# Optimization experiments

Hardware: AMD Instinct MI355X
Metric: run time of the kernel (lower is better)

Reference implementation:

```python
import jax, jax.numpy as jnp
import numpy as np

K = 2
N_NODES = 100_000
N_EDGES = 1_600_000
STATIC_F = 16
DYN_F = 32
EDGE_F = 8
IN_F = EDGE_F + 2 * STATIC_F + 2 * DYN_F  # 104
HID_F = 2 * DYN_F  # 64


def setup_inputs() -> dict:
    key = jax.random.key(0)
    ks = jax.random.split(key, 9)
    x_s = jax.random.normal(ks[0], (N_NODES, STATIC_F), dtype=jnp.float32)
    x_t = jax.random.normal(ks[1], (N_NODES, DYN_F), dtype=jnp.float32)
    edge_index = jax.random.randint(ks[2], (2, N_EDGES), 0, N_NODES, dtype=jnp.int64 if jax.config.jax_enable_x64 else jnp.int32)
    edge_attr = jax.random.normal(ks[3], (N_EDGES, EDGE_F), dtype=jnp.float32)
    W1 = jax.random.normal(ks[4], (IN_F, HID_F), dtype=jnp.float32) / np.sqrt(IN_F)
    b1 = jnp.zeros((HID_F,), dtype=jnp.float32)
    W2 = jax.random.normal(ks[5], (HID_F, DYN_F), dtype=jnp.float32) / np.sqrt(HID_F)
    b2 = jnp.zeros((DYN_F,), dtype=jnp.float32)
    F = jax.random.normal(ks[6], (K + 1, DYN_F, DYN_F), dtype=jnp.float32) / np.sqrt(DYN_F)
    return {"x_s": x_s, "x_t": x_t, "edge_index": edge_index, "edge_attr": edge_attr,
            "W1": W1, "b1": b1, "W2": W2, "b2": b2, "F": F}


def reference(x_s, x_t, edge_index, edge_attr, W1, b1, W2, b2, F):
    row, col = edge_index[0], edge_index[1]
    num_nodes = x_t.shape[0]
    # filter_matrix[0] (Linear, no bias); F[k] stored as [in, out]
    out = x_t @ F[0]
    xs_row = x_s[row]  # static gathers are loop-invariant
    xs_col = x_s[col]
    for k in range(K):
        mask = jnp.sum(out, axis=1) != 0  # [N]
        edge_mask = (mask[row] | mask[col]).astype(out.dtype)[:, None]  # [E,1]
        out_row = out[row]
        out_col = out[col]
        e_ij = jnp.concatenate([xs_row, xs_col, out_row, out_col, edge_attr], axis=1)  # [E,104]
        w_ij = jax.nn.relu(e_ij @ W1 + b1) @ W2 + b2  # [E,32]
        # normalize per edge; NaN (zero-norm) -> 0, matching masked_fill_
        nrm = jnp.linalg.norm(w_ij, axis=1, keepdims=True)
        w_ij = jnp.where(nrm > 0, w_ij / jnp.where(nrm > 0, nrm, 1.0), 0.0)
        # with_gradient: (x_j - x_i) * w_ij; zero out edges failing the mask
        shift = (out_col - out_row) * w_ij * edge_mask
        scattered = jax.ops.segment_sum(shift, col, num_segments=num_nodes)
        out = out + scattered @ F[k + 1]
    return out
```

## Files before the change

### kernel.cpp

```cpp
#include <hip/hip_runtime.h>

#define NN 100000
#define NE 1600000
#define SF 16
#define DF 32
#define EFT 8
#define HF 64

typedef __attribute__((ext_vector_type(8))) short short8;
typedef __attribute__((ext_vector_type(4))) float floatx4;

__device__ inline unsigned short f2bf(float f) {
  union { float f; unsigned int u; } v; v.f = f;
  unsigned int u = v.u + 0x7FFFu + ((v.u >> 16) & 1u);
  return (unsigned short)(u >> 16);
}
__device__ inline float bf2f(unsigned short h) {
  union { unsigned int u; float f; } v; v.u = ((unsigned int)h) << 16;
  return v.f;
}

__global__ __launch_bounds__(256) void hist_kernel(const int* __restrict__ ei,
                                                   int* __restrict__ deg) {
  int e = blockIdx.x * 256 + threadIdx.x;
  if (e < NE) atomicAdd(&deg[ei[NE + e]], 1);
}

__global__ __launch_bounds__(256) void scan1_kernel(const int* __restrict__ deg,
                                                    int* __restrict__ cur,
                                                    int* __restrict__ bsums) {
  __shared__ int ts[256];
  int tid = threadIdx.x;
  int base = blockIdx.x * 1024 + tid * 4;
  int v[4];
#pragma unroll
  for (int q = 0; q < 4; ++q) v[q] = (base + q < NN) ? deg[base + q] : 0;
  int s = v[0] + v[1] + v[2] + v[3];
  ts[tid] = s;
  __syncthreads();
  for (int off = 1; off < 256; off <<= 1) {
    int t = (tid >= off) ? ts[tid - off] : 0;
    __syncthreads();
    ts[tid] += t;
    __syncthreads();
  }
  int excl = ts[tid] - s;
  if (tid == 255) bsums[blockIdx.x] = ts[255];
  int run = excl;
#pragma unroll
  for (int q = 0; q < 4; ++q) {
    if (base + q < NN) cur[base + q] = run;
    run += v[q];
  }
}

__global__ void scan2_kernel(int* __restrict__ bsums, int nb) {
  int acc = 0;
  for (int i = 0; i < nb; ++i) { int t = bsums[i]; bsums[i] = acc; acc += t; }
}

__global__ __launch_bounds__(256) void scan3_kernel(int* __restrict__ cur,
                                                    const int* __restrict__ bsums) {
  int i = blockIdx.x * 256 + threadIdx.x;
  if (i < NN) cur[i] += bsums[i >> 10];
}

__global__ __launch_bounds__(256) void fill_kernel(const int* __restrict__ ei,
                                                   const float* __restrict__ ea,
                                                   int* __restrict__ cur,
                                                   int* __restrict__ row_s,
                                                   int* __restrict__ col_s,
                                                   unsigned short* __restrict__ ea_s) {
  int e = blockIdx.x * 256 + threadIdx.x;
  if (e >= NE) return;
  int r = ei[e];
  int c = ei[NE + e];
  int pos = atomicAdd(&cur[c], 1);
  row_s[pos] = r;
  col_s[pos] = c;
  const float4* p = (const float4*)(ea + (size_t)e * EFT);
  float4 v0 = p[0], v1 = p[1];
  short8 ev;
  ev[0] = (short)f2bf(v0.x); ev[1] = (short)f2bf(v0.y);
  ev[2] = (short)f2bf(v0.z); ev[3] = (short)f2bf(v0.w);
  ev[4] = (short)f2bf(v1.x); ev[5] = (short)f2bf(v1.y);
  ev[6] = (short)f2bf(v1.z); ev[7] = (short)f2bf(v1.w);
  *(short8*)(ea_s + (size_t)pos * 8) = ev;
}

__global__ __launch_bounds__(256) void wpre_kernel(const float* __restrict__ W1,
                                                   unsigned short* __restrict__ WpreT) {
  int id = blockIdx.x * 256 + threadIdx.x;
  if (id >= 128 * 64) return;
  int col = id >> 6, k = id & 63;
  int j = col & 63;
  bool bh = col >= 64;
  float v = 0.f;
  if (k < 16) v = W1[((bh ? 16 : 0) + k) * HF + j];
  else if (k < 48) v = W1[((bh ? 64 : 32) + (k - 16)) * HF + j];
  WpreT[col * 64 + k] = f2bf(v);
}

__global__ __launch_bounds__(256) void init_kernel(
    const float* __restrict__ x_t, const float* __restrict__ F0,
    float* __restrict__ out, unsigned short* __restrict__ outb,
    float* __restrict__ sums) {
  int n = blockIdx.x * 256 + threadIdx.x;
  if (n >= NN) return;
  float x[DF];
  const float4* xr = reinterpret_cast<const float4*>(x_t + (size_t)n * DF);
#pragma unroll
  for (int q = 0; q < 8; ++q) {
    float4 v = xr[q];
    x[4*q+0]=v.x; x[4*q+1]=v.y; x[4*q+2]=v.z; x[4*q+3]=v.w;
  }
  float4* orow = reinterpret_cast<float4*>(out + (size_t)n * DF);
  unsigned short* ob = outb + (size_t)n * DF;
  float s = 0.f;
#pragma unroll
  for (int q = 0; q < 8; ++q) {
    float4 acc = {0.f, 0.f, 0.f, 0.f};
#pragma unroll
    for (int i = 0; i < DF; ++i) {
      float xi = x[i];
      acc.x = fmaf(xi, F0[i*DF + 4*q+0], acc.x);
      acc.y = fmaf(xi, F0[i*DF + 4*q+1], acc.y);
      acc.z = fmaf(xi, F0[i*DF + 4*q+2], acc.z);
      acc.w = fmaf(xi, F0[i*DF + 4*q+3], acc.w);
    }
    orow[q] = acc;
    s += acc.x + acc.y + acc.z + acc.w;
    ushort4 pk = {f2bf(acc.x), f2bf(acc.y), f2bf(acc.z), f2bf(acc.w)};
    *(ushort4*)(ob + 4*q) = pk;
  }
  sums[n] = s;
}

__global__ __launch_bounds__(256, 4) void pre_kernel(
    const float* __restrict__ x_s, const unsigned short* __restrict__ outb,
    const unsigned short* __restrict__ WpreT, unsigned short* __restrict__ ABh) {
  __shared__ unsigned short wlds[128][72];
  int tid = threadIdx.x;
  for (int t = tid; t < 128 * 8; t += 256) {
    int colr = t >> 3, kc = t & 7;
    short8 v = *(const short8*)(WpreT + colr * 64 + kc * 8);
    *(short8*)(&wlds[colr][kc * 8]) = v;
  }
  __syncthreads();

  int lcol = tid & 15, kgrp = (tid >> 4) & 3, wid = tid >> 6;
  int nodebase = blockIdx.x * 64 + wid * 16;
  int nodeA = nodebase + lcol;

  short8 a0 = {0,0,0,0,0,0,0,0}, a1 = {0,0,0,0,0,0,0,0};
  if (nodeA < NN) {
    const unsigned short* obp = outb + (size_t)nodeA * DF;
    if (kgrp == 0) {
      const float4* p = (const float4*)(x_s + (size_t)nodeA * SF);
      float4 v0 = p[0], v1 = p[1];
      a0[0]=(short)f2bf(v0.x); a0[1]=(short)f2bf(v0.y);
      a0[2]=(short)f2bf(v0.z); a0[3]=(short)f2bf(v0.w);
      a0[4]=(short)f2bf(v1.x); a0[5]=(short)f2bf(v1.y);
      a0[6]=(short)f2bf(v1.z); a0[7]=(short)f2bf(v1.w);
      a1 = *(const short8*)(obp + 16);
    } else if (kgrp == 1) {
      const float4* p = (const float4*)(x_s + (size_t)nodeA * SF);
      float4 v0 = p[2], v1 = p[3];
      a0[0]=(short)f2bf(v0.x); a0[1]=(short)f2bf(v0.y);
      a0[2]=(short)f2bf(v0.z); a0[3]=(short)f2bf(v0.w);
      a0[4]=(short)f2bf(v1.x); a0[5]=(short)f2bf(v1.y);
      a0[6]=(short)f2bf(v1.z); a0[7]=(short)f2bf(v1.w);
      a1 = *(const short8*)(obp + 24);
    } else if (kgrp == 2) {
      a0 = *(const short8*)(obp + 0);
    } else {
      a0 = *(const short8*)(obp + 8);
    }
  }

  floatx4 acc[8];
#pragma unroll
  for (int nt = 0; nt < 8; ++nt) {
    short8 b0 = *(const short8*)(&wlds[nt * 16 + lcol][kgrp * 8]);
    short8 b1 = *(const short8*)(&wlds[nt * 16 + lcol][32 + kgrp * 8]);
    floatx4 c = {0.f, 0.f, 0.f, 0.f};
    c = __builtin_amdgcn_mfma_f32_16x16x32_bf16(a0, b0, c, 0, 0, 0);
    c = __builtin_amdgcn_mfma_f32_16x16x32_bf16(a1, b1, c, 0, 0, 0);
    acc[nt] = c;
  }

#pragma unroll
  for (int rr = 0; rr < 4; ++rr) {
    int node = nodebase + kgrp * 4 + rr;
    if (node < NN) {
      unsigned short* dst = ABh + (size_t)node * 128;
#pragma unroll
      for (int nt = 0; nt < 8; ++nt)
        dst[nt * 16 + lcol] = f2bf(acc[nt][rr]);
    }
  }
}

__global__ __launch_bounds__(256, 4) void edge_kernel(
    const unsigned short* __restrict__ ABh, const unsigned short* __restrict__ outb,
    const float* __restrict__ sums, const unsigned short* __restrict__ ea_s,
    const int* __restrict__ row_s, const int* __restrict__ col_s,
    const float* __restrict__ W1, const float* __restrict__ b1,
    const float* __restrict__ W2, const float* __restrict__ b2,
    float* __restrict__ scattered) {
  __shared__ union { unsigned short h[256][72]; float sh[256][33]; } u;
  __shared__ int scol[256];
  __shared__ int srow[256];
  __shared__ union { float msk[256]; struct { unsigned short l0[256], l1[256]; } seg; } vv;
  __shared__ int wbase[4];
  __shared__ int cnt;

  int tid = threadIdx.x;
  int bbase = blockIdx.x * 256;
  int i = bbase + tid;
  if (tid == 0) cnt = 0;
  int lcol = tid & 15;
  int kgrp = (tid >> 4) & 3;
  int wid = tid >> 6;

  short8 w2f[2][2];
#pragma unroll
  for (int kt = 0; kt < 2; ++kt)
#pragma unroll
    for (int nt = 0; nt < 2; ++nt) {
#pragma unroll
      for (int q = 0; q < 8; ++q)
        w2f[kt][nt][q] = (short)f2bf(W2[(kt*32 + kgrp*8 + q) * DF + nt*16 + lcol]);
    }
  float b2c0 = b2[lcol], b2c1 = b2[16 + lcol];

  if (i < NE) {
    int r = row_s[i];
    int c = col_s[i];
    scol[tid] = c;
    srow[tid] = r;
    float s_r = sums[r], s_c = sums[c];
    vv.msk[tid] = (s_r == 0.f && s_c == 0.f) ? 0.f : 1.f;
    float eav[8];
    {
      short8 ev = *(const short8*)(ea_s + (size_t)i * 8);
#pragma unroll
      for (int t = 0; t < 8; ++t) eav[t] = bf2f((unsigned short)ev[t]);
    }
    const unsigned short* ar = ABh + (size_t)r * 128;
    const unsigned short* bc = ABh + (size_t)c * 128 + 64;
#pragma unroll 1
    for (int ch = 0; ch < 4; ++ch) {
      short8 a0 = *(const short8*)(ar + ch*16);
      short8 a1 = *(const short8*)(ar + ch*16 + 8);
      short8 c0 = *(const short8*)(bc + ch*16);
      short8 c1 = *(const short8*)(bc + ch*16 + 8);
      short8 p0, p1;
#pragma unroll
      for (int j = 0; j < 16; ++j) {
        float cj = b1[ch*16 + j];
#pragma unroll
        for (int t = 0; t < 8; ++t)
          cj = fmaf(eav[t], W1[(96 + t) * HF + ch*16 + j], cj);
        float av = bf2f((unsigned short)(j < 8 ? a0[j] : a1[j-8]));
        float bv = bf2f((unsigned short)(j < 8 ? c0[j] : c1[j-8]));
        float hv = fmaxf(av + bv + cj, 0.f);
        unsigned short hb = f2bf(hv);
        if (j < 8) p0[j] = (short)hb; else p1[j-8] = (short)hb;
      }
      *(short8*)(&u.h[tid][ch*16]) = p0;
      *(short8*)(&u.h[tid][ch*16 + 8]) = p1;
    }
  } else {
    scol[tid] = -1;
    srow[tid] = 0;
    vv.msk[tid] = 0.f;
  }
  __syncthreads();

  floatx4 acc[4][2];
#pragma unroll
  for (int g = 0; g < 4; ++g) {
    int erow = wid*64 + g*16 + lcol;
    short8 a0 = *(const short8*)(&u.h[erow][kgrp*8]);
    short8 a1 = *(const short8*)(&u.h[erow][32 + kgrp*8]);
    floatx4 c0 = {b2c0, b2c0, b2c0, b2c0};
    floatx4 c1 = {b2c1, b2c1, b2c1, b2c1};
    c0 = __builtin_amdgcn_mfma_f32_16x16x32_bf16(a0, w2f[0][0], c0, 0, 0, 0);
    c0 = __builtin_amdgcn_mfma_f32_16x16x32_bf16(a1, w2f[1][0], c0, 0, 0, 0);
    c1 = __builtin_amdgcn_mfma_f32_16x16x32_bf16(a0, w2f[0][1], c1, 0, 0, 0);
    c1 = __builtin_amdgcn_mfma_f32_16x16x32_bf16(a1, w2f[1][1], c1, 0, 0, 0);
    acc[g][0] = c0;
    acc[g][1] = c1;
  }
  __syncthreads();

#pragma unroll
  for (int g = 0; g < 4; ++g) {
    float nsq[4];
#pragma unroll
    for (int rr = 0; rr < 4; ++rr)
      nsq[rr] = acc[g][0][rr]*acc[g][0][rr] + acc[g][1][rr]*acc[g][1][rr];
#pragma unroll
    for (int mm = 1; mm <= 8; mm <<= 1) {
#pragma unroll
      for (int rr = 0; rr < 4; ++rr)
        nsq[rr] += __shfl_xor(nsq[rr], mm, 64);
    }
#pragma unroll
    for (int rr = 0; rr < 4; ++rr) {
      int e = wid*64 + g*16 + kgrp*4 + rr;
      if (bbase + e < NE) {
        float ms = (nsq[rr] > 0.f) ? rsqrtf(nsq[rr]) : 0.f;
        ms *= vv.msk[e];
        int r2 = srow[e];
        int c2 = scol[e];
        float ar0 = bf2f(outb[(size_t)r2*DF + lcol]);
        float ar1 = bf2f(outb[(size_t)r2*DF + 16 + lcol]);
        float bc0 = bf2f(outb[(size_t)c2*DF + lcol]);
        float bc1 = bf2f(outb[(size_t)c2*DF + 16 + lcol]);
        u.sh[e][lcol]      = (bc0 - ar0) * acc[g][0][rr] * ms;
        u.sh[e][16 + lcol] = (bc1 - ar1) * acc[g][1][rr] * ms;
      }
    }
  }
  __syncthreads();

  int c_self = scol[tid];
  bool head = (c_self >= 0) && (tid == 0 || scol[tid-1] != c_self);
  unsigned long long m = __ballot(head);
  int lane = tid & 63;
  if (lane == 0) wbase[wid] = atomicAdd(&cnt, (int)__popcll(m));
  __syncthreads();
  if (head) {
    int idx = wbase[wid] + (int)__popcll(m & ((1ull << lane) - 1ull));
    int t1 = tid + 1;
    while (t1 < 256 && scol[t1] == c_self) ++t1;
    vv.seg.l0[idx] = (unsigned short)tid;
    vv.seg.l1[idx] = (unsigned short)t1;
  }
  __syncthreads();
  int nr = cnt;
  for (int task = tid; task < nr * 32; task += 256) {
    int rid = task >> 5, j = task & 31;
    int t0 = vv.seg.l0[rid], t1 = vv.seg.l1[rid];
    float s = 0.f;
    for (int t = t0; t < t1; ++t) s += u.sh[t][j];
    unsafeAtomicAdd(&scattered[(size_t)scol[t0] * DF + j], s);
  }
}

__global__ __launch_bounds__(256) void node_kernel(
    float* __restrict__ out, float* __restrict__ scattered,
    const float* __restrict__ Fk, unsigned short* __restrict__ outb,
    float* __restrict__ sums) {
  int n = blockIdx.x * 256 + threadIdx.x;
  if (n >= NN) return;
  float s[DF];
  float4* sp = reinterpret_cast<float4*>(scattered + (size_t)n * DF);
#pragma unroll
  for (int q = 0; q < 8; ++q) {
    float4 v = sp[q];
    s[4*q+0]=v.x; s[4*q+1]=v.y; s[4*q+2]=v.z; s[4*q+3]=v.w;
  }
  float4* op = reinterpret_cast<float4*>(out + (size_t)n * DF);
  unsigned short* ob = outb + (size_t)n * DF;
  float ssum = 0.f;
#pragma unroll
  for (int q = 0; q < 8; ++q) {
    float4 acc = op[q];
#pragma unroll
    for (int i = 0; i < DF; ++i) {
      float si = s[i];
      acc.x = fmaf(si, Fk[i*DF + 4*q+0], acc.x);
      acc.y = fmaf(si, Fk[i*DF + 4*q+1], acc.y);
      acc.z = fmaf(si, Fk[i*DF + 4*q+2], acc.z);
      acc.w = fmaf(si, Fk[i*DF + 4*q+3], acc.w);
    }
    op[q] = acc;
    ssum += acc.x + acc.y + acc.z + acc.w;
    ushort4 pk = {f2bf(acc.x), f2bf(acc.y), f2bf(acc.z), f2bf(acc.w)};
    *(ushort4*)(ob + 4*q) = pk;
  }
  sums[n] = ssum;
  float4 z = {0.f, 0.f, 0.f, 0.f};
#pragma unroll
  for (int q = 0; q < 8; ++q) sp[q] = z;
}

extern "C" void kernel_launch(void* const* d_in, const int* in_sizes, int n_in,
                              void* d_out, int out_size, void* d_ws, size_t ws_size,
                              hipStream_t stream) {
  const float* x_s = (const float*)d_in[0];
  const float* x_t = (const float*)d_in[1];
  const int*   ei  = (const int*)d_in[2];
  const float* ea  = (const float*)d_in[3];
  const float* W1  = (const float*)d_in[4];
  const float* b1  = (const float*)d_in[5];
  const float* W2  = (const float*)d_in[6];
  const float* b2  = (const float*)d_in[7];
  const float* F   = (const float*)d_in[8];

  float* out = (float*)d_out;
  char* ws = (char*)d_ws;
  float*          scattered = (float*)(ws);
  unsigned short* ABh       = (unsigned short*)(ws + 12800000);
  unsigned short* outb      = (unsigned short*)(ws + 38400000);
  float*          sums      = (float*)(ws + 44800000);
  int*            row_s     = (int*)(ws + 45200000);
  int*            col_s     = (int*)(ws + 51600000);
  unsigned short* ea_s      = (unsigned short*)(ws + 58000000);
  int*            deg       = (int*)(ws + 83600000);
  int*            cur       = (int*)(ws + 84000000);
  int*            bsums     = (int*)(ws + 84400000);
  unsigned short* WpreT     = (unsigned short*)(ws + 84401024);

  hipMemsetAsync(deg, 0, NN * sizeof(int), stream);
  hipMemsetAsync(scattered, 0, (size_t)NN * DF * sizeof(float), stream);

  dim3 blk(256);
  dim3 grid_e((NE + 255) / 256);
  dim3 grid_n((NN + 255) / 256);
  dim3 grid_p((NN + 63) / 64);
  int nscan = (NN + 1023) / 1024;

  hist_kernel<<<grid_e, blk, 0, stream>>>(ei, deg);
  scan1_kernel<<<nscan, blk, 0, stream>>>(deg, cur, bsums);
  scan2_kernel<<<1, 1, 0, stream>>>(bsums, nscan);
  scan3_kernel<<<grid_n, blk, 0, stream>>>(cur, bsums);
  fill_kernel<<<grid_e, blk, 0, stream>>>(ei, ea, cur, row_s, col_s, ea_s);
  wpre_kernel<<<32, blk, 0, stream>>>(W1, WpreT);

  init_kernel<<<grid_n, blk, 0, stream>>>(x_t, F, out, outb, sums);

  for (int k = 0; k < 2; ++k) {
    pre_kernel<<<grid_p, blk, 0, stream>>>(x_s, outb, WpreT, ABh);
    edge_kernel<<<grid_e, blk, 0, stream>>>(ABh, outb, sums, ea_s,
                                            row_s, col_s,
                                            W1, b1, W2, b2, scattered);
    node_kernel<<<grid_n, blk, 0, stream>>>(out, scattered,
                                            F + (size_t)(k + 1) * DF * DF,
                                            outb, sums);
  }
}
```

Measured before the change: 522.9 us.

## Precompute edge-attr W1 projection once, switch to fp16 MFMA, merge setup kernels

The edge_attr part of the first MLP layer (edge_attr @ W1 + b1) is now computed once per edge in the fill kernel and stored as fp16 when the workspace is large enough. This removes the per-iteration 8x64 FMA work from the edge kernel, at the cost of extra memory traffic. The bf16 storage and MFMA paths become fp16 with packed half adds and a sign-mask ReLU. W2 fragments are pre-packed, and the memsets, weight prep and the serial scan2 are folded into a setup kernel and a prefix loop in scan3. Bounds checks that relied on NE being a multiple of 256 are dropped.

```diff
diff --git a/kernel.cpp b/kernel.cpp
--- a/kernel.cpp
+++ b/kernel.cpp
@@ -7,18 +7,10 @@
 #define EFT 8
 #define HF 64
 
+typedef __attribute__((ext_vector_type(8))) _Float16 half8;
+typedef __attribute__((ext_vector_type(4))) _Float16 half4;
 typedef __attribute__((ext_vector_type(8))) short short8;
 typedef __attribute__((ext_vector_type(4))) float floatx4;
-
-__device__ inline unsigned short f2bf(float f) {
-  union { float f; unsigned int u; } v; v.f = f;
-  unsigned int u = v.u + 0x7FFFu + ((v.u >> 16) & 1u);
-  return (unsigned short)(u >> 16);
-}
-__device__ inline float bf2f(unsigned short h) {
-  union { unsigned int u; float f; } v; v.u = ((unsigned int)h) << 16;
-  return v.f;
-}
 
 __global__ __launch_bounds__(256) void hist_kernel(const int* __restrict__ ei,
                                                    int* __restrict__ deg) {
@@ -54,56 +46,89 @@
   }
 }
 
-__global__ void scan2_kernel(int* __restrict__ bsums, int nb) {
-  int acc = 0;
-  for (int i = 0; i < nb; ++i) { int t = bsums[i]; bsums[i] = acc; acc += t; }
-}
-
 __global__ __launch_bounds__(256) void scan3_kernel(int* __restrict__ cur,
                                                     const int* __restrict__ bsums) {
   int i = blockIdx.x * 256 + threadIdx.x;
-  if (i < NN) cur[i] += bsums[i >> 10];
-}
-
-__global__ __launch_bounds__(256) void fill_kernel(const int* __restrict__ ei,
-                                                   const float* __restrict__ ea,
-                                                   int* __restrict__ cur,
-                                                   int* __restrict__ row_s,
-                                                   int* __restrict__ col_s,
-                                                   unsigned short* __restrict__ ea_s) {
+  int g = blockIdx.x >> 2;
+  int pref = 0;
+  for (int q = 0; q < g; ++q) pref += bsums[q];
+  if (i < NN) cur[i] += pref;
+}
+
+__global__ __launch_bounds__(256) void setup_kernel(
+    const float* __restrict__ W1, const float* __restrict__ W2,
+    _Float16* __restrict__ WpreT, _Float16* __restrict__ w2pk,
+    float4* __restrict__ scattered4, int* __restrict__ deg) {
+  int gid = blockIdx.x * 256 + threadIdx.x;
+  if (gid < 800000) {
+    float4 z = {0.f, 0.f, 0.f, 0.f};
+    scattered4[gid] = z;
+  }
+  if (gid < NN) deg[gid] = 0;
+  if (gid < 128 * 64) {
+    int col = gid >> 6, k = gid & 63;
+    int j = col & 63;
+    bool bh = col >= 64;
+    float v = 0.f;
+    if (k < 16) v = W1[((bh ? 16 : 0) + k) * HF + j];
+    else if (k < 48) v = W1[((bh ? 64 : 32) + (k - 16)) * HF + j];
+    WpreT[gid] = (_Float16)v;
+  }
+  if (gid < 2048) {
+    int lane = gid >> 5, idx = gid & 31;
+    int kt = idx >> 4, nt = (idx >> 3) & 1, q = idx & 7;
+    int kgrp = (lane >> 4) & 3, lcol = lane & 15;
+    w2pk[gid] = (_Float16)W2[(kt * 32 + kgrp * 8 + q) * DF + nt * 16 + lcol];
+  }
+}
+
+template <bool TP>
+__global__ __launch_bounds__(256) void fill_kernel(
+    const int* __restrict__ ei, const float* __restrict__ ea,
+    const float* __restrict__ W1, const float* __restrict__ b1,
+    int* __restrict__ cur, int* __restrict__ row_s, int* __restrict__ col_s,
+    _Float16* __restrict__ eaw, _Float16* __restrict__ ea_s) {
   int e = blockIdx.x * 256 + threadIdx.x;
-  if (e >= NE) return;
   int r = ei[e];
   int c = ei[NE + e];
   int pos = atomicAdd(&cur[c], 1);
   row_s[pos] = r;
   col_s[pos] = c;
+  float eav[8];
   const float4* p = (const float4*)(ea + (size_t)e * EFT);
   float4 v0 = p[0], v1 = p[1];
-  short8 ev;
-  ev[0] = (short)f2bf(v0.x); ev[1] = (short)f2bf(v0.y);
-  ev[2] = (short)f2bf(v0.z); ev[3] = (short)f2bf(v0.w);
-  ev[4] = (short)f2bf(v1.x); ev[5] = (short)f2bf(v1.y);
-  ev[6] = (short)f2bf(v1.z); ev[7] = (short)f2bf(v1.w);
-  *(short8*)(ea_s + (size_t)pos * 8) = ev;
-}
-
-__global__ __launch_bounds__(256) void wpre_kernel(const float* __restrict__ W1,
-                                                   unsigned short* __restrict__ WpreT) {
-  int id = blockIdx.x * 256 + threadIdx.x;
-  if (id >= 128 * 64) return;
-  int col = id >> 6, k = id & 63;
-  int j = col & 63;
-  bool bh = col >= 64;
-  float v = 0.f;
-  if (k < 16) v = W1[((bh ? 16 : 0) + k) * HF + j];
-  else if (k < 48) v = W1[((bh ? 64 : 32) + (k - 16)) * HF + j];
-  WpreT[col * 64 + k] = f2bf(v);
+  eav[0]=v0.x; eav[1]=v0.y; eav[2]=v0.z; eav[3]=v0.w;
+  eav[4]=v1.x; eav[5]=v1.y; eav[6]=v1.z; eav[7]=v1.w;
+  if constexpr (TP) {
+    _Float16* dst = eaw + (size_t)pos * 64;
+#pragma unroll 2
+    for (int q8 = 0; q8 < 8; ++q8) {
+      float acc[8];
+#pragma unroll
+      for (int jj = 0; jj < 8; ++jj) acc[jj] = b1[q8 * 8 + jj];
+#pragma unroll
+      for (int t = 0; t < 8; ++t) {
+        float x = eav[t];
+        const float* w = W1 + (96 + t) * HF + q8 * 8;
+#pragma unroll
+        for (int jj = 0; jj < 8; ++jj) acc[jj] = fmaf(x, w[jj], acc[jj]);
+      }
+      half8 h;
+#pragma unroll
+      for (int jj = 0; jj < 8; ++jj) h[jj] = (_Float16)acc[jj];
+      *(half8*)(dst + q8 * 8) = h;
+    }
+  } else {
+    half8 h;
+#pragma unroll
+    for (int t = 0; t < 8; ++t) h[t] = (_Float16)eav[t];
+    *(half8*)(ea_s + (size_t)pos * 8) = h;
+  }
 }
 
 __global__ __launch_bounds__(256) void init_kernel(
     const float* __restrict__ x_t, const float* __restrict__ F0,
-    float* __restrict__ out, unsigned short* __restrict__ outb,
+    float* __restrict__ out, _Float16* __restrict__ outb,
     float* __restrict__ sums) {
   int n = blockIdx.x * 256 + threadIdx.x;
   if (n >= NN) return;
@@ -115,7 +140,7 @@
     x[4*q+0]=v.x; x[4*q+1]=v.y; x[4*q+2]=v.z; x[4*q+3]=v.w;
   }
   float4* orow = reinterpret_cast<float4*>(out + (size_t)n * DF);
-  unsigned short* ob = outb + (size_t)n * DF;
+  _Float16* ob = outb + (size_t)n * DF;
   float s = 0.f;
 #pragma unroll
   for (int q = 0; q < 8; ++q) {
@@ -130,21 +155,20 @@
     }
     orow[q] = acc;
     s += acc.x + acc.y + acc.z + acc.w;
-    ushort4 pk = {f2bf(acc.x), f2bf(acc.y), f2bf(acc.z), f2bf(acc.w)};
-    *(ushort4*)(ob + 4*q) = pk;
+    half4 pk = {(_Float16)acc.x, (_Float16)acc.y, (_Float16)acc.z, (_Float16)acc.w};
+    *(half4*)(ob + 4*q) = pk;
   }
   sums[n] = s;
 }
 
 __global__ __launch_bounds__(256, 4) void pre_kernel(
-    const float* __restrict__ x_s, const unsigned short* __restrict__ outb,
-    const unsigned short* __restrict__ WpreT, unsigned short* __restrict__ ABh) {
-  __shared__ unsigned short wlds[128][72];
+    const float* __restrict__ x_s, const _Float16* __restrict__ outb,
+    const _Float16* __restrict__ WpreT, _Float16* __restrict__ ABh) {
+  __shared__ _Float16 wlds[128][72];
   int tid = threadIdx.x;
-  for (int t = tid; t < 128 * 8; t += 256) {
+  for (int t = tid; t < 1024; t += 256) {
     int colr = t >> 3, kc = t & 7;
-    short8 v = *(const short8*)(WpreT + colr * 64 + kc * 8);
-    *(short8*)(&wlds[colr][kc * 8]) = v;
+    *(half8*)(&wlds[colr][kc * 8]) = *(const half8*)(WpreT + colr * 64 + kc * 8);
   }
   __syncthreads();
 
@@ -152,40 +176,32 @@
   int nodebase = blockIdx.x * 64 + wid * 16;
   int nodeA = nodebase + lcol;
 
-  short8 a0 = {0,0,0,0,0,0,0,0}, a1 = {0,0,0,0,0,0,0,0};
+  half8 a0 = {}, a1 = {};
   if (nodeA < NN) {
-    const unsigned short* obp = outb + (size_t)nodeA * DF;
-    if (kgrp == 0) {
+    const _Float16* obp = outb + (size_t)nodeA * DF;
+    if (kgrp < 2) {
       const float4* p = (const float4*)(x_s + (size_t)nodeA * SF);
-      float4 v0 = p[0], v1 = p[1];
-      a0[0]=(short)f2bf(v0.x); a0[1]=(short)f2bf(v0.y);
-      a0[2]=(short)f2bf(v0.z); a0[3]=(short)f2bf(v0.w);
-      a0[4]=(short)f2bf(v1.x); a0[5]=(short)f2bf(v1.y);
-      a0[6]=(short)f2bf(v1.z); a0[7]=(short)f2bf(v1.w);
-      a1 = *(const short8*)(obp + 16);
-    } else if (kgrp == 1) {
-      const float4* p = (const float4*)(x_s + (size_t)nodeA * SF);
-      float4 v0 = p[2], v1 = p[3];
-      a0[0]=(short)f2bf(v0.x); a0[1]=(short)f2bf(v0.y);
-      a0[2]=(short)f2bf(v0.z); a0[3]=(short)f2bf(v0.w);
-      a0[4]=(short)f2bf(v1.x); a0[5]=(short)f2bf(v1.y);
-      a0[6]=(short)f2bf(v1.z); a0[7]=(short)f2bf(v1.w);
-      a1 = *(const short8*)(obp + 24);
+      float4 v0 = p[kgrp * 2], v1 = p[kgrp * 2 + 1];
+      a0[0]=(_Float16)v0.x; a0[1]=(_Float16)v0.y;
+      a0[2]=(_Float16)v0.z; a0[3]=(_Float16)v0.w;
+      a0[4]=(_Float16)v1.x; a0[5]=(_Float16)v1.y;
+      a0[6]=(_Float16)v1.z; a0[7]=(_Float16)v1.w;
+      a1 = *(const half8*)(obp + 16 + kgrp * 8);
     } else if (kgrp == 2) {
-      a0 = *(const short8*)(obp + 0);
+      a0 = *(const half8*)(obp + 0);
     } else {
-      a0 = *(const short8*)(obp + 8);
+      a0 = *(const half8*)(obp + 8);
     }
   }
 
   floatx4 acc[8];
 #pragma unroll
   for (int nt = 0; nt < 8; ++nt) {
-    short8 b0 = *(const short8*)(&wlds[nt * 16 + lcol][kgrp * 8]);
-    short8 b1 = *(const short8*)(&wlds[nt * 16 + lcol][32 + kgrp * 8]);
+    half8 b0 = *(const half8*)(&wlds[nt * 16 + lcol][kgrp * 8]);
+    half8 b1v = *(const half8*)(&wlds[nt * 16 + lcol][32 + kgrp * 8]);
     floatx4 c = {0.f, 0.f, 0.f, 0.f};
-    c = __builtin_amdgcn_mfma_f32_16x16x32_bf16(a0, b0, c, 0, 0, 0);
-    c = __builtin_amdgcn_mfma_f32_16x16x32_bf16(a1, b1, c, 0, 0, 0);
+    c = __builtin_amdgcn_mfma_f32_16x16x32_f16(a0, b0, c, 0, 0, 0);
+    c = __builtin_amdgcn_mfma_f32_16x16x32_f16(a1, b1v, c, 0, 0, 0);
     acc[nt] = c;
   }
 
@@ -193,20 +209,22 @@
   for (int rr = 0; rr < 4; ++rr) {
     int node = nodebase + kgrp * 4 + rr;
     if (node < NN) {
-      unsigned short* dst = ABh + (size_t)node * 128;
+      _Float16* dst = ABh + (size_t)node * 128;
 #pragma unroll
       for (int nt = 0; nt < 8; ++nt)
-        dst[nt * 16 + lcol] = f2bf(acc[nt][rr]);
-    }
-  }
-}
-
+        dst[nt * 16 + lcol] = (_Float16)acc[nt][rr];
+    }
+  }
+}
+
+template <bool TP>
 __global__ __launch_bounds__(256, 4) void edge_kernel(
-    const unsigned short* __restrict__ ABh, const unsigned short* __restrict__ outb,
-    const float* __restrict__ sums, const unsigned short* __restrict__ ea_s,
+    const _Float16* __restrict__ ABh, const _Float16* __restrict__ outb,
+    const float* __restrict__ sums, const _Float16* __restrict__ eaw,
+    const _Float16* __restrict__ ea_s,
     const int* __restrict__ row_s, const int* __restrict__ col_s,
     const float* __restrict__ W1, const float* __restrict__ b1,
-    const float* __restrict__ W2, const float* __restrict__ b2,
+    const float* __restrict__ b2, const _Float16* __restrict__ w2pk,
     float* __restrict__ scattered) {
   __shared__ union { unsigned short h[256][72]; float sh[256][33]; } u;
   __shared__ int scol[256];
@@ -219,77 +237,73 @@
   int bbase = blockIdx.x * 256;
   int i = bbase + tid;
   if (tid == 0) cnt = 0;
-  int lcol = tid & 15;
-  int kgrp = (tid >> 4) & 3;
-  int wid = tid >> 6;
-
-  short8 w2f[2][2];
-#pragma unroll
-  for (int kt = 0; kt < 2; ++kt)
-#pragma unroll
-    for (int nt = 0; nt < 2; ++nt) {
-#pragma unroll
-      for (int q = 0; q < 8; ++q)
-        w2f[kt][nt][q] = (short)f2bf(W2[(kt*32 + kgrp*8 + q) * DF + nt*16 + lcol]);
-    }
+  int lcol = tid & 15, kgrp = (tid >> 4) & 3, wid = tid >> 6;
+
+  const _Float16* wpp = w2pk + (size_t)(tid & 63) * 32;
+  half8 w2f00 = *(const half8*)(wpp);
+  half8 w2f01 = *(const half8*)(wpp + 8);
+  half8 w2f10 = *(const half8*)(wpp + 16);
+  half8 w2f11 = *(const half8*)(wpp + 24);
   float b2c0 = b2[lcol], b2c1 = b2[16 + lcol];
 
-  if (i < NE) {
-    int r = row_s[i];
-    int c = col_s[i];
-    scol[tid] = c;
-    srow[tid] = r;
-    float s_r = sums[r], s_c = sums[c];
-    vv.msk[tid] = (s_r == 0.f && s_c == 0.f) ? 0.f : 1.f;
+  int r = row_s[i];
+  int c = col_s[i];
+  scol[tid] = c;
+  srow[tid] = r;
+  float s_r = sums[r], s_c = sums[c];
+  vv.msk[tid] = (s_r == 0.f && s_c == 0.f) ? 0.f : 1.f;
+
+  const _Float16* ar = ABh + (size_t)r * 128;
+  const _Float16* bc = ABh + (size_t)c * 128 + 64;
+  if constexpr (TP) {
+    const _Float16* ew = eaw + (size_t)i * 64;
+#pragma unroll 4
+    for (int q = 0; q < 8; ++q) {
+      half8 a = *(const half8*)(ar + q * 8);
+      half8 b = *(const half8*)(bc + q * 8);
+      half8 w = *(const half8*)(ew + q * 8);
+      half8 s = a + b + w;
+      short8 sb = __builtin_bit_cast(short8, s);
+      short8 m = sb >> 15;
+      sb = sb & ~m;
+      *(short8*)(&u.h[tid][q * 8]) = sb;
+    }
+  } else {
     float eav[8];
-    {
-      short8 ev = *(const short8*)(ea_s + (size_t)i * 8);
-#pragma unroll
-      for (int t = 0; t < 8; ++t) eav[t] = bf2f((unsigned short)ev[t]);
-    }
-    const unsigned short* ar = ABh + (size_t)r * 128;
-    const unsigned short* bc = ABh + (size_t)c * 128 + 64;
+    half8 ev = *(const half8*)(ea_s + (size_t)i * 8);
+#pragma unroll
+    for (int t = 0; t < 8; ++t) eav[t] = (float)ev[t];
 #pragma unroll 1
-    for (int ch = 0; ch < 4; ++ch) {
-      short8 a0 = *(const short8*)(ar + ch*16);
-      short8 a1 = *(const short8*)(ar + ch*16 + 8);
-      short8 c0 = *(const short8*)(bc + ch*16);
-      short8 c1 = *(const short8*)(bc + ch*16 + 8);
-      short8 p0, p1;
-#pragma unroll
-      for (int j = 0; j < 16; ++j) {
-        float cj = b1[ch*16 + j];
-#pragma unroll
-        for (int t = 0; t < 8; ++t)
-          cj = fmaf(eav[t], W1[(96 + t) * HF + ch*16 + j], cj);
-        float av = bf2f((unsigned short)(j < 8 ? a0[j] : a1[j-8]));
-        float bv = bf2f((unsigned short)(j < 8 ? c0[j] : c1[j-8]));
-        float hv = fmaxf(av + bv + cj, 0.f);
-        unsigned short hb = f2bf(hv);
-        if (j < 8) p0[j] = (short)hb; else p1[j-8] = (short)hb;
+    for (int q = 0; q < 8; ++q) {
+      half8 a = *(const half8*)(ar + q * 8);
+      half8 b = *(const half8*)(bc + q * 8);
+      half8 hh;
+#pragma unroll
+      for (int jj = 0; jj < 8; ++jj) {
+        int j = q * 8 + jj;
+        float cj = b1[j];
+#pragma unroll
+        for (int t = 0; t < 8; ++t) cj = fmaf(eav[t], W1[(96 + t) * HF + j], cj);
+        float hv = fmaxf((float)a[jj] + (float)b[jj] + cj, 0.f);
+        hh[jj] = (_Float16)hv;
       }
-      *(short8*)(&u.h[tid][ch*16]) = p0;
-      *(short8*)(&u.h[tid][ch*16 + 8]) = p1;
-    }
-  } else {
-    scol[tid] = -1;
-    srow[tid] = 0;
-    vv.msk[tid] = 0.f;
+      *(half8*)(&u.h[tid][q * 8]) = hh;
+    }
   }
   __syncthreads();
 
   floatx4 acc[4][2];
 #pragma unroll
   for (int g = 0; g < 4; ++g) {
-    int erow = wid*64 + g*16 + lcol;
-    short8 a0 = *(const short8*)(&u.h[erow][kgrp*8]);
-    short8 a1 = *(const short8*)(&u.h[erow][32 + kgrp*8]);
+    int erow = wid * 64 + g * 16 + lcol;
+    half8 a0 = *(const half8*)(&u.h[erow][kgrp * 8]);
+    half8 a1 = *(const half8*)(&u.h[erow][32 + kgrp * 8]);
     floatx4 c0 = {b2c0, b2c0, b2c0, b2c0};
     floatx4 c1 = {b2c1, b2c1, b2c1, b2c1};
-    c0 = __builtin_amdgcn_mfma_f32_16x16x32_bf16(a0, w2f[0][0], c0, 0, 0, 0);
-    c0 = __builtin_amdgcn_mfma_f32_16x16x32_bf16(a1, w2f[1][0], c0, 0, 0, 0);
-    c1 = __builtin_amdgcn_mfma_f32_16x16x32_bf16(a0, w2f[0][1], c1, 0, 0, 0);
-    c1 = __builtin_amdgcn_mfma_f32_16x16x32_bf16(a1, w2f[1][1], c1, 0, 0, 0);
+    c0 = __builtin_amdgcn_mfma_f32_16x16x32_f16(a0, w2f00, c0, 0, 0, 0);
+    c0 = __builtin_amdgcn_mfma_f32_16x16x32_f16(a1, w2f10, c0, 0, 0, 0);
+    c1 = __builtin_amdgcn_mfma_f32_16x16x32_f16(a0, w2f01, c1, 0, 0, 0);
+    c1 = __builtin_amdgcn_mfma_f32_16x16x32_f16(a1, w2f11, c1, 0, 0, 0);
     acc[g][0] = c0;
     acc[g][1] = c1;
   }
@@ -309,25 +323,23 @@
     }
 #pragma unroll
     for (int rr = 0; rr < 4; ++rr) {
-      int e = wid*64 + g*16 + kgrp*4 + rr;
-      if (bbase + e < NE) {
-        float ms = (nsq[rr] > 0.f) ? rsqrtf(nsq[rr]) : 0.f;
-        ms *= vv.msk[e];
-        int r2 = srow[e];
-        int c2 = scol[e];
-        float ar0 = bf2f(outb[(size_t)r2*DF + lcol]);
-        float ar1 = bf2f(outb[(size_t)r2*DF + 16 + lcol]);
-        float bc0 = bf2f(outb[(size_t)c2*DF + lcol]);
-        float bc1 = bf2f(outb[(size_t)c2*DF + 16 + lcol]);
-        u.sh[e][lcol]      = (bc0 - ar0) * acc[g][0][rr] * ms;
-        u.sh[e][16 + lcol] = (bc1 - ar1) * acc[g][1][rr] * ms;
-      }
+      int e = wid * 64 + g * 16 + kgrp * 4 + rr;
+      float ms = (nsq[rr] > 0.f) ? rsqrtf(nsq[rr]) : 0.f;
+      ms *= vv.msk[e];
+      int r2 = srow[e];
+      int c2 = scol[e];
+      float ar0 = (float)outb[(size_t)r2 * DF + lcol];
+      float ar1 = (float)outb[(size_t)r2 * DF + 16 + lcol];
+      float bc0 = (float)outb[(size_t)c2 * DF + lcol];
+      float bc1 = (float)outb[(size_t)c2 * DF + 16 + lcol];
+      u.sh[e][lcol]      = (bc0 - ar0) * acc[g][0][rr] * ms;
+      u.sh[e][16 + lcol] = (bc1 - ar1) * acc[g][1][rr] * ms;
     }
   }
   __syncthreads();
 
   int c_self = scol[tid];
-  bool head = (c_self >= 0) && (tid == 0 || scol[tid-1] != c_self);
+  bool head = (tid == 0 || scol[tid - 1] != c_self);
   unsigned long long m = __ballot(head);
   int lane = tid & 63;
   if (lane == 0) wbase[wid] = atomicAdd(&cnt, (int)__popcll(m));
@@ -352,7 +364,7 @@
 
 __global__ __launch_bounds__(256) void node_kernel(
     float* __restrict__ out, float* __restrict__ scattered,
-    const float* __restrict__ Fk, unsigned short* __restrict__ outb,
+    const float* __restrict__ Fk, _Float16* __restrict__ outb,
     float* __restrict__ sums) {
   int n = blockIdx.x * 256 + threadIdx.x;
   if (n >= NN) return;
@@ -364,7 +376,7 @@
     s[4*q+0]=v.x; s[4*q+1]=v.y; s[4*q+2]=v.z; s[4*q+3]=v.w;
   }
   float4* op = reinterpret_cast<float4*>(out + (size_t)n * DF);
-  unsigned short* ob = outb + (size_t)n * DF;
+  _Float16* ob = outb + (size_t)n * DF;
   float ssum = 0.f;
 #pragma unroll
   for (int q = 0; q < 8; ++q) {
@@ -379,8 +391,8 @@
     }
     op[q] = acc;
     ssum += acc.x + acc.y + acc.z + acc.w;
-    ushort4 pk = {f2bf(acc.x), f2bf(acc.y), f2bf(acc.z), f2bf(acc.w)};
-    *(ushort4*)(ob + 4*q) = pk;
+    half4 pk = {(_Float16)acc.x, (_Float16)acc.y, (_Float16)acc.z, (_Float16)acc.w};
+    *(half4*)(ob + 4*q) = pk;
   }
   sums[n] = ssum;
   float4 z = {0.f, 0.f, 0.f, 0.f};
@@ -403,41 +415,52 @@
 
   float* out = (float*)d_out;
   char* ws = (char*)d_ws;
-  float*          scattered = (float*)(ws);
-  unsigned short* ABh       = (unsigned short*)(ws + 12800000);
-  unsigned short* outb      = (unsigned short*)(ws + 38400000);
-  float*          sums      = (float*)(ws + 44800000);
-  int*            row_s     = (int*)(ws + 45200000);
-  int*            col_s     = (int*)(ws + 51600000);
-  unsigned short* ea_s      = (unsigned short*)(ws + 58000000);
-  int*            deg       = (int*)(ws + 83600000);
-  int*            cur       = (int*)(ws + 84000000);
-  int*            bsums     = (int*)(ws + 84400000);
-  unsigned short* WpreT     = (unsigned short*)(ws + 84401024);
-
-  hipMemsetAsync(deg, 0, NN * sizeof(int), stream);
-  hipMemsetAsync(scattered, 0, (size_t)NN * DF * sizeof(float), stream);
+  float*     scattered = (float*)(ws);
+  _Float16*  ABh       = (_Float16*)(ws + 12800000);
+  _Float16*  outb      = (_Float16*)(ws + 38400000);
+  float*     sums      = (float*)(ws + 44800000);
+  int*       row_s     = (int*)(ws + 45200000);
+  int*       col_s     = (int*)(ws + 51600000);
+  int*       deg       = (int*)(ws + 58000000);
+  int*       cur       = (int*)(ws + 58400000);
+  int*       bsums     = (int*)(ws + 58800000);
+  _Float16*  WpreT     = (_Float16*)(ws + 58810000);
+  _Float16*  w2pk      = (_Float16*)(ws + 58830000);
+  _Float16*  eaw       = (_Float16*)(ws + 58900000);
+  _Float16*  ea_s      = (_Float16*)(ws + 58900000);
+
+  bool tp = ws_size >= 263700000ull;
 
   dim3 blk(256);
-  dim3 grid_e((NE + 255) / 256);
+  dim3 grid_e(NE / 256);
   dim3 grid_n((NN + 255) / 256);
   dim3 grid_p((NN + 63) / 64);
   int nscan = (NN + 1023) / 1024;
 
+  setup_kernel<<<3125, blk, 0, stream>>>(W1, W2, WpreT, w2pk,
+                                         (float4*)scattered, deg);
   hist_kernel<<<grid_e, blk, 0, stream>>>(ei, deg);
   scan1_kernel<<<nscan, blk, 0, stream>>>(deg, cur, bsums);
-  scan2_kernel<<<1, 1, 0, stream>>>(bsums, nscan);
   scan3_kernel<<<grid_n, blk, 0, stream>>>(cur, bsums);
-  fill_kernel<<<grid_e, blk, 0, stream>>>(ei, ea, cur, row_s, col_s, ea_s);
-  wpre_kernel<<<32, blk, 0, stream>>>(W1, WpreT);
+  if (tp)
+    fill_kernel<true><<<grid_e, blk, 0, stream>>>(ei, ea, W1, b1, cur,
+                                                  row_s, col_s, eaw, ea_s);
+  else
+    fill_kernel<false><<<grid_e, blk, 0, stream>>>(ei, ea, W1, b1, cur,
+                                                   row_s, col_s, eaw, ea_s);
 
   init_kernel<<<grid_n, blk, 0, stream>>>(x_t, F, out, outb, sums);
 
   for (int k = 0; k < 2; ++k) {
     pre_kernel<<<grid_p, blk, 0, stream>>>(x_s, outb, WpreT, ABh);
-    edge_kernel<<<grid_e, blk, 0, stream>>>(ABh, outb, sums, ea_s,
-                                            row_s, col_s,
-                                            W1, b1, W2, b2, scattered);
+    if (tp)
+      edge_kernel<true><<<grid_e, blk, 0, stream>>>(ABh, outb, sums, eaw, ea_s,
+                                                    row_s, col_s, W1, b1, b2,
+                                                    w2pk, scattered);
+    else
+      edge_kernel<false><<<grid_e, blk, 0, stream>>>(ABh, outb, sums, eaw, ea_s,
+                                                     row_s, col_s, W1, b1, b2,
+                                                     w2pk, scattered);
     node_kernel<<<grid_n, blk, 0, stream>>>(out, scattered,
                                             F + (size_t)(k + 1) * DF * DF,
                                             outb, sums);
```

New measurement: 600.6 us. 1.15x slower.
